# Kernel tuning notes

Hardware: AMD Instinct MI355X
Metric: run time of the kernel (lower is better)

## Reference

```python
import jax, jax.numpy as jnp
import numpy as np

HEADS = 8
DIM_HEAD = 64
DIM_INNER = HEADS * DIM_HEAD  # 512
SCALE = DIM_HEAD ** -0.5
B, N, D = 8, 512, 512
NEG = -1e9


def setup_inputs() -> dict:
    key = jax.random.key(0)
    ks = jax.random.split(key, 12)
    inp = {}
    for i in range(3):
        inp[f"x{i}"] = jax.random.normal(ks[i], (B, N, D), dtype=jnp.float32)
        inp[f"m{i}"] = jax.random.randint(ks[3 + i], (B, N), 0, 2).astype(bool)
        inp[f"Wqkv{i}"] = jax.random.normal(ks[6 + i], (D, 3 * DIM_INNER), dtype=jnp.float32) * 0.02
        inp[f"Wout{i}"] = jax.random.normal(ks[9 + i], (DIM_INNER, D), dtype=jnp.float32) * 0.02
    return inp


def _split_heads(t):
    # [b, n, h*d] -> [b, h, n, d]
    b, n, _ = t.shape
    return t.reshape(b, n, HEADS, DIM_HEAD).transpose(0, 2, 1, 3)


def _forward(xs, masks, Wqkvs, Wouts):
    qs, ks, vs = [], [], []
    for x, W in zip(xs, Wqkvs):
        q, k, v = jnp.split(x @ W, 3, axis=-1)
        qs.append(_split_heads(q))
        ks.append(_split_heads(k))
        vs.append(_split_heads(v))
    K = jnp.concatenate(ks, axis=2)  # [b, h, 3n, d]
    V = jnp.concatenate(vs, axis=2)
    outs = []
    for q, m, Wo in zip(qs, masks, Wouts):
        dots = jnp.einsum('bhnd,bhmd->bhnm', q, K) * SCALE
        # original masks whole query rows: masked_fill(~mask[:, None, :, None], -1e9)
        dots = jnp.where(m[:, None, :, None], dots, NEG)
        attn = jax.nn.softmax(dots, axis=-1)  # dropout is identity at eval
        o = jnp.einsum('bhnm,bhmd->bhnd', attn, V)
        o = o.transpose(0, 2, 1, 3).reshape(q.shape[0], q.shape[2], DIM_INNER)
        outs.append(o @ Wo)
    return tuple(outs)


def reference(x0, x1, x2, m0, m1, m2, Wqkv0, Wqkv1, Wqkv2, Wout0, Wout1, Wout2):
    return _forward((x0, x1, x2), (m0, m1, m2), (Wqkv0, Wqkv1, Wqkv2), (Wout0, Wout1, Wout2))
```

## Files before the change

### kernel.cpp

```cpp
#include <hip/hip_runtime.h>
#include <cstdint>
#include <cstddef>

#define NEGV  -1.0e9f
#define QSCALE 0.18033688011112042f

typedef _Float16 h8 __attribute__((ext_vector_type(8)));
typedef _Float16 h4 __attribute__((ext_vector_type(4)));
typedef float    f4 __attribute__((ext_vector_type(4)));


static __device__ inline h8 cvt8(float4 a, float4 b) {
    h8 r = { (_Float16)a.x, (_Float16)a.y, (_Float16)a.z, (_Float16)a.w,
             (_Float16)b.x, (_Float16)b.y, (_Float16)b.z, (_Float16)b.w };
    return r;
}

__global__ __launch_bounds__(256) void tr_cvt(
    const float* __restrict__ s0, const float* __restrict__ s1, const float* __restrict__ s2,
    _Float16* __restrict__ dst, int R, int C)
{
    const int mod = blockIdx.z;
    const float* __restrict__ s = (mod == 0) ? s0 : ((mod == 1) ? s1 : s2);
    _Float16* __restrict__ d = dst + (size_t)mod * R * C;
    const int c0 = blockIdx.x * 32, r0 = blockIdx.y * 32;
    __shared__ float tile[32][33];
    const int tr = threadIdx.x >> 3;
    const int tc = (threadIdx.x & 7) * 4;
    float4 v = *reinterpret_cast<const float4*>(&s[(size_t)(r0 + tr) * C + c0 + tc]);
    tile[tr][tc + 0] = v.x; tile[tr][tc + 1] = v.y; tile[tr][tc + 2] = v.z; tile[tr][tc + 3] = v.w;
    __syncthreads();
    h4 o = { (_Float16)tile[tc + 0][tr], (_Float16)tile[tc + 1][tr],
             (_Float16)tile[tc + 2][tr], (_Float16)tile[tc + 3][tr] };
    *reinterpret_cast<h4*>(&d[(size_t)(c0 + tr) * R + r0 + tc]) = o;
}

__global__ __launch_bounds__(256) void qkv_gemm_f16(
    const float* __restrict__ x0, const float* __restrict__ x1, const float* __restrict__ x2,
    const _Float16* __restrict__ Wqt,
    _Float16* __restrict__ Qh, _Float16* __restrict__ Kh, _Float16* __restrict__ Vt)
{
    const int mod = blockIdx.z;
    const float* __restrict__ A = (mod == 0) ? x0 : ((mod == 1) ? x1 : x2);
    const _Float16* __restrict__ Bw = Wqt + (size_t)mod * 1536 * 512;

    __shared__ _Float16 smem[2 * 128 * 40];
    _Float16* As = smem;
    _Float16* Bs = smem + 128 * 40;

    const int t = threadIdx.x;
    const int brow = blockIdx.x * 128, bcol = blockIdx.y * 128;
    const int w = t >> 6, l = t & 63;
    const int wr = (w >> 1) * 64, wc = (w & 1) * 64;
    const int lr = l & 15, lk = (l >> 4) * 8, lg = l >> 4;

    const int sm0 = t >> 2, skk = (t & 3) * 8, sm1 = sm0 + 64;

    f4 acc[4][4] = {};
    float4 axr[2][2];
    h8 brg[2];

    axr[0][0] = *reinterpret_cast<const float4*>(&A[(size_t)(brow + sm0) * 512 + skk]);
    axr[0][1] = *reinterpret_cast<const float4*>(&A[(size_t)(brow + sm0) * 512 + skk + 4]);
    axr[1][0] = *reinterpret_cast<const float4*>(&A[(size_t)(brow + sm1) * 512 + skk]);
    axr[1][1] = *reinterpret_cast<const float4*>(&A[(size_t)(brow + sm1) * 512 + skk + 4]);
    brg[0] = *reinterpret_cast<const h8*>(&Bw[(size_t)(bcol + sm0) * 512 + skk]);
    brg[1] = *reinterpret_cast<const h8*>(&Bw[(size_t)(bcol + sm1) * 512 + skk]);
    *reinterpret_cast<h8*>(&As[sm0 * 40 + skk]) = cvt8(axr[0][0], axr[0][1]);
    *reinterpret_cast<h8*>(&As[sm1 * 40 + skk]) = cvt8(axr[1][0], axr[1][1]);
    *reinterpret_cast<h8*>(&Bs[sm0 * 40 + skk]) = brg[0];
    *reinterpret_cast<h8*>(&Bs[sm1 * 40 + skk]) = brg[1];

    for (int k0 = 0; k0 < 512; k0 += 32) {
        __syncthreads();
        const bool more = (k0 + 32) < 512;
        if (more) {
            const int kn = k0 + 32 + skk;
            axr[0][0] = *reinterpret_cast<const float4*>(&A[(size_t)(brow + sm0) * 512 + kn]);
            axr[0][1] = *reinterpret_cast<const float4*>(&A[(size_t)(brow + sm0) * 512 + kn + 4]);
            axr[1][0] = *reinterpret_cast<const float4*>(&A[(size_t)(brow + sm1) * 512 + kn]);
            axr[1][1] = *reinterpret_cast<const float4*>(&A[(size_t)(brow + sm1) * 512 + kn + 4]);
            brg[0] = *reinterpret_cast<const h8*>(&Bw[(size_t)(bcol + sm0) * 512 + k0 + 32 + skk]);
            brg[1] = *reinterpret_cast<const h8*>(&Bw[(size_t)(bcol + sm1) * 512 + k0 + 32 + skk]);
        }
        h8 af[4], bf[4];
#pragma unroll
        for (int m = 0; m < 4; m++)
            af[m] = *reinterpret_cast<h8*>(&As[(wr + m * 16 + lr) * 40 + lk]);
#pragma unroll
        for (int n = 0; n < 4; n++)
            bf[n] = *reinterpret_cast<h8*>(&Bs[(wc + n * 16 + lr) * 40 + lk]);
        __builtin_amdgcn_s_setprio(1);
#pragma unroll
        for (int m = 0; m < 4; m++)
#pragma unroll
            for (int n = 0; n < 4; n++)
                acc[m][n] = __builtin_amdgcn_mfma_f32_16x16x32_f16(af[m], bf[n], acc[m][n], 0, 0, 0);
        __builtin_amdgcn_s_setprio(0);
        __syncthreads();
        if (more) {
            *reinterpret_cast<h8*>(&As[sm0 * 40 + skk]) = cvt8(axr[0][0], axr[0][1]);
            *reinterpret_cast<h8*>(&As[sm1 * 40 + skk]) = cvt8(axr[1][0], axr[1][1]);
            *reinterpret_cast<h8*>(&Bs[sm0 * 40 + skk]) = brg[0];
            *reinterpret_cast<h8*>(&Bs[sm1 * 40 + skk]) = brg[1];
        }
    }

    const int sec = bcol >> 9;
    const int b = brow >> 9;
    const int nbase = brow & 511;
    const int cbase = bcol - (sec << 9);

    if (sec == 2) {
#pragma unroll
        for (int m = 0; m < 4; m++) {
            const int n = nbase + wr + m * 16 + lg * 4;
#pragma unroll
            for (int nn = 0; nn < 4; nn++) {
                const int cis = cbase + wc + nn * 16 + lr;
                const int hh = cis >> 6, d = cis & 63;
                h4 pv = { (_Float16)acc[m][nn][0], (_Float16)acc[m][nn][1],
                          (_Float16)acc[m][nn][2], (_Float16)acc[m][nn][3] };
                *reinterpret_cast<h4*>(&Vt[(((size_t)b * 8 + hh) * 64 + d) * 1536 + mod * 512 + n]) = pv;
            }
        }
    } else {
        const float scl = (sec == 0) ? QSCALE : 1.0f;
        _Float16 (*Ts)[136] = reinterpret_cast<_Float16(*)[136]>(smem);
#pragma unroll
        for (int pass = 0; pass < 2; pass++) {
            __syncthreads();
            if ((w >> 1) == pass) {
#pragma unroll
                for (int m = 0; m < 4; m++)
#pragma unroll
                    for (int nn = 0; nn < 4; nn++)
#pragma unroll
                        for (int reg = 0; reg < 4; reg++)
                            Ts[m * 16 + lg * 4 + reg][wc + nn * 16 + lr] =
                                (_Float16)(acc[m][nn][reg] * scl);
            }
            __syncthreads();
#pragma unroll
            for (int it = 0; it < 4; it++) {
                const int idx = t + it * 256;
                const int r = idx >> 4, c = (idx & 15) * 8;
                h8 v = *reinterpret_cast<h8*>(&Ts[r][c]);
                const int n = nbase + pass * 64 + r;
                const int cis = cbase + c;
                const int hh = cis >> 6, d = cis & 63;
                if (sec == 0)
                    *reinterpret_cast<h8*>(&Qh[((((size_t)mod * 8 + b) * 8 + hh) * 512 + n) * 64 + d]) = v;
                else
                    *reinterpret_cast<h8*>(&Kh[(((size_t)b * 8 + hh) * 1536 + mod * 512 + n) * 64 + d]) = v;
            }
        }
    }
}

__global__ __launch_bounds__(512) void attn_f16(
    const _Float16* __restrict__ Qh, const _Float16* __restrict__ Kh, const _Float16* __restrict__ Vt,
    const int* __restrict__ m0, const int* __restrict__ m1, const int* __restrict__ m2,
    _Float16* __restrict__ Oh)
{
    const int mod = blockIdx.z;
    const int bh = blockIdx.x, b = bh >> 3, h = bh & 7;
    const int q0 = blockIdx.y * 128;

    __shared__ _Float16 Ks[64 * 72];
    __shared__ _Float16 Vs[64 * 72];
    __shared__ _Float16 Ps[128 * 72];

    const int t = threadIdx.x, w = t >> 6, l = t & 63;
    const int lr = l & 15, lg = l >> 4, lk = lg * 8;

    const _Float16* __restrict__ Qp = Qh + ((((size_t)mod * 8 + b) * 8 + h) * 512 + q0 + w * 16) * 64;
    h8 qf0 = *reinterpret_cast<const h8*>(&Qp[(size_t)lr * 64 + lk]);
    h8 qf1 = *reinterpret_cast<const h8*>(&Qp[(size_t)lr * 64 + 32 + lk]);

    const int* __restrict__ mk = (mod == 0) ? m0 : ((mod == 1) ? m1 : m2);
    const bool msk = mk[b * 512 + q0 + w * 16 + lr] != 0;

    float mrow = -3.0e38f, lsum = 0.f;
    f4 o[4] = {};

    const int sr = t >> 3, skk = (t & 7) * 8;
    const _Float16* __restrict__ kSrc = Kh + (size_t)bh * 1536 * 64 + (size_t)sr * 64 + skk;
    const _Float16* __restrict__ vSrc = Vt + (size_t)bh * 64 * 1536 + (size_t)sr * 1536 + skk;
    _Float16* kDst = &Ks[sr * 72 + skk];
    _Float16* vDst = &Vs[sr * 72 + skk];

    h8 krg = *reinterpret_cast<const h8*>(kSrc);
    h8 vrg = *reinterpret_cast<const h8*>(vSrc);
    *reinterpret_cast<h8*>(kDst) = krg;
    *reinterpret_cast<h8*>(vDst) = vrg;

    for (int c0 = 0; c0 < 1536; c0 += 64) {
        __syncthreads();
        const bool more = (c0 + 64) < 1536;
        if (more) {
            krg = *reinterpret_cast<const h8*>(kSrc + (size_t)(c0 + 64) * 64);
            vrg = *reinterpret_cast<const h8*>(vSrc + (c0 + 64));
        }

        f4 st[4] = {};
        __builtin_amdgcn_s_setprio(1);
#pragma unroll
        for (int kb = 0; kb < 4; kb++) {
            h8 ka0 = *reinterpret_cast<h8*>(&Ks[(kb * 16 + lr) * 72 + lk]);
            h8 ka1 = *reinterpret_cast<h8*>(&Ks[(kb * 16 + lr) * 72 + 32 + lk]);
            st[kb] = __builtin_amdgcn_mfma_f32_16x16x32_f16(ka0, qf0, st[kb], 0, 0, 0);
            st[kb] = __builtin_amdgcn_mfma_f32_16x16x32_f16(ka1, qf1, st[kb], 0, 0, 0);
        }
        __builtin_amdgcn_s_setprio(0);

        if (!msk) {
#pragma unroll
            for (int kb = 0; kb < 4; kb++) { st[kb][0] = NEGV; st[kb][1] = NEGV; st[kb][2] = NEGV; st[kb][3] = NEGV; }
        }
        float cm = fmaxf(fmaxf(fmaxf(st[0][0], st[0][1]), fmaxf(st[0][2], st[0][3])),
                         fmaxf(fmaxf(st[1][0], st[1][1]), fmaxf(st[1][2], st[1][3])));
        cm = fmaxf(cm, fmaxf(fmaxf(fmaxf(st[2][0], st[2][1]), fmaxf(st[2][2], st[2][3])),
                             fmaxf(fmaxf(st[3][0], st[3][1]), fmaxf(st[3][2], st[3][3]))));
        cm = fmaxf(cm, __shfl_xor(cm, 16));
        cm = fmaxf(cm, __shfl_xor(cm, 32));

        if (!__all(cm <= mrow + 8.0f)) {
            const float mn = fmaxf(mrow, cm);
            const float sc = __builtin_amdgcn_exp2f(mrow - mn);
            mrow = mn;
            lsum *= sc;
#pragma unroll
            for (int dg = 0; dg < 4; dg++) o[dg] *= sc;
        }

        float rs = 0.f;
#pragma unroll
        for (int kb = 0; kb < 4; kb++) {
            const float p0 = __builtin_amdgcn_exp2f(st[kb][0] - mrow);
            const float p1 = __builtin_amdgcn_exp2f(st[kb][1] - mrow);
            const float p2 = __builtin_amdgcn_exp2f(st[kb][2] - mrow);
            const float p3 = __builtin_amdgcn_exp2f(st[kb][3] - mrow);
            rs += (p0 + p1) + (p2 + p3);
            h4 ph = { (_Float16)p0, (_Float16)p1, (_Float16)p2, (_Float16)p3 };
            *reinterpret_cast<h4*>(&Ps[(w * 16 + lr) * 72 + kb * 16 + lg * 4]) = ph;
        }
        rs += __shfl_xor(rs, 16);
        rs += __shfl_xor(rs, 32);
        lsum += rs;

        __builtin_amdgcn_s_setprio(1);
#pragma unroll
        for (int kb2 = 0; kb2 < 2; kb2++) {
            h8 pa = *reinterpret_cast<h8*>(&Ps[(w * 16 + lr) * 72 + kb2 * 32 + lk]);
#pragma unroll
            for (int dg = 0; dg < 4; dg++) {
                h8 va = *reinterpret_cast<h8*>(&Vs[(dg * 16 + lr) * 72 + kb2 * 32 + lk]);
                o[dg] = __builtin_amdgcn_mfma_f32_16x16x32_f16(va, pa, o[dg], 0, 0, 0);
            }
        }
        __builtin_amdgcn_s_setprio(0);

        __syncthreads();
        if (more) {
            *reinterpret_cast<h8*>(kDst) = krg;
            *reinterpret_cast<h8*>(vDst) = vrg;
        }
    }

    const float inv = 1.f / lsum;
    const size_t row = (size_t)mod * 4096 + b * 512 + q0 + w * 16 + lr;
#pragma unroll
    for (int dg = 0; dg < 4; dg++) {
        h4 ov = { (_Float16)(o[dg][0] * inv), (_Float16)(o[dg][1] * inv),
                  (_Float16)(o[dg][2] * inv), (_Float16)(o[dg][3] * inv) };
        *reinterpret_cast<h4*>(&Oh[row * 512 + h * 64 + dg * 16 + lg * 4]) = ov;
    }
}

__global__ __launch_bounds__(256) void out_gemm_f16(
    const _Float16* __restrict__ Oh, const _Float16* __restrict__ Wot,
    float* __restrict__ out)
{
    const int mod = blockIdx.z;
    const _Float16* __restrict__ A  = Oh  + (size_t)mod * 4096 * 512;
    const _Float16* __restrict__ Bw = Wot + (size_t)mod * 512 * 512;
    float* __restrict__ C = out + (size_t)mod * 4096 * 512;

    __shared__ _Float16 As[128 * 40];
    __shared__ _Float16 Bs[128 * 40];

    const int t = threadIdx.x;
    const int brow = blockIdx.x * 128, bcol = blockIdx.y * 128;
    const int w = t >> 6, l = t & 63;
    const int wr = (w >> 1) * 64, wc = (w & 1) * 64;
    const int lr = l & 15, lk = (l >> 4) * 8, lg = l >> 4;

    const int sm0 = t >> 2, skk = (t & 3) * 8, sm1 = sm0 + 64;

    f4 acc[4][4] = {};
    h8 arg[2], brg[2];

    arg[0] = *reinterpret_cast<const h8*>(&A [(size_t)(brow + sm0) * 512 + skk]);
    arg[1] = *reinterpret_cast<const h8*>(&A [(size_t)(brow + sm1) * 512 + skk]);
    brg[0] = *reinterpret_cast<const h8*>(&Bw[(size_t)(bcol + sm0) * 512 + skk]);
    brg[1] = *reinterpret_cast<const h8*>(&Bw[(size_t)(bcol + sm1) * 512 + skk]);
    *reinterpret_cast<h8*>(&As[sm0 * 40 + skk]) = arg[0];
    *reinterpret_cast<h8*>(&As[sm1 * 40 + skk]) = arg[1];
    *reinterpret_cast<h8*>(&Bs[sm0 * 40 + skk]) = brg[0];
    *reinterpret_cast<h8*>(&Bs[sm1 * 40 + skk]) = brg[1];

    for (int k0 = 0; k0 < 512; k0 += 32) {
        __syncthreads();
        const bool more = (k0 + 32) < 512;
        if (more) {
            const int kn = k0 + 32 + skk;
            arg[0] = *reinterpret_cast<const h8*>(&A [(size_t)(brow + sm0) * 512 + kn]);
            arg[1] = *reinterpret_cast<const h8*>(&A [(size_t)(brow + sm1) * 512 + kn]);
            brg[0] = *reinterpret_cast<const h8*>(&Bw[(size_t)(bcol + sm0) * 512 + kn]);
            brg[1] = *reinterpret_cast<const h8*>(&Bw[(size_t)(bcol + sm1) * 512 + kn]);
        }
        h8 af[4], bf[4];
#pragma unroll
        for (int m = 0; m < 4; m++)
            af[m] = *reinterpret_cast<h8*>(&As[(wr + m * 16 + lr) * 40 + lk]);
#pragma unroll
        for (int n = 0; n < 4; n++)
            bf[n] = *reinterpret_cast<h8*>(&Bs[(wc + n * 16 + lr) * 40 + lk]);
        __builtin_amdgcn_s_setprio(1);
#pragma unroll
        for (int m = 0; m < 4; m++)
#pragma unroll
            for (int n = 0; n < 4; n++)
                acc[m][n] = __builtin_amdgcn_mfma_f32_16x16x32_f16(af[m], bf[n], acc[m][n], 0, 0, 0);
        __builtin_amdgcn_s_setprio(0);
        __syncthreads();
        if (more) {
            *reinterpret_cast<h8*>(&As[sm0 * 40 + skk]) = arg[0];
            *reinterpret_cast<h8*>(&As[sm1 * 40 + skk]) = arg[1];
            *reinterpret_cast<h8*>(&Bs[sm0 * 40 + skk]) = brg[0];
            *reinterpret_cast<h8*>(&Bs[sm1 * 40 + skk]) = brg[1];
        }
    }

#pragma unroll
    for (int m = 0; m < 4; m++) {
        const int rloc = wr + m * 16 + lg * 4;
#pragma unroll
        for (int reg = 0; reg < 4; reg++) {
            const size_t base = (size_t)(brow + rloc + reg) * 512 + bcol;
#pragma unroll
            for (int nn = 0; nn < 4; nn++)
                C[base + wc + nn * 16 + lr] = acc[m][nn][reg];
        }
    }
}

extern "C" void kernel_launch(void* const* d_in, const int* in_sizes, int n_in,
                              void* d_out, int out_size, void* d_ws, size_t ws_size,
                              hipStream_t stream)
{
    const float* x0  = (const float*)d_in[0];
    const int*   m0  = (const int*)  d_in[1];
    const float* Wq0 = (const float*)d_in[2];
    const float* Wo0 = (const float*)d_in[3];
    const float* x1  = (const float*)d_in[4];
    const int*   m1  = (const int*)  d_in[5];
    const float* Wq1 = (const float*)d_in[6];
    const float* Wo1 = (const float*)d_in[7];
    const float* x2  = (const float*)d_in[8];
    const int*   m2  = (const int*)  d_in[9];
    const float* Wq2 = (const float*)d_in[10];
    const float* Wo2 = (const float*)d_in[11];

    _Float16* Wqt = (_Float16*)d_ws;
    _Float16* Wot = Wqt + 2359296;
    _Float16* Qh  = Wot + 786432;
    _Float16* Kh  = Qh  + 6291456;
    _Float16* Vt  = Kh  + 6291456;
    _Float16* Oh  = Vt  + 6291456;

    tr_cvt<<<dim3(48, 16, 3), 256, 0, stream>>>(Wq0, Wq1, Wq2, Wqt, 512, 1536);
    tr_cvt<<<dim3(16, 16, 3), 256, 0, stream>>>(Wo0, Wo1, Wo2, Wot, 512, 512);

    qkv_gemm_f16<<<dim3(32, 12, 3), 256, 0, stream>>>(x0, x1, x2, Wqt, Qh, Kh, Vt);
    attn_f16    <<<dim3(64, 4, 3), 512, 0, stream>>>(Qh, Kh, Vt, m0, m1, m2, Oh);
    out_gemm_f16<<<dim3(32, 4, 3), 256, 0, stream>>>(Oh, Wot, (float*)d_out);
}
```

Measured before the change: 230.7 us.

## Coalesce V and output stores via LDS, merge weight converts, shrink attention blocks

```diff
diff --git a/kernel.cpp b/kernel.cpp
--- a/kernel.cpp
+++ b/kernel.cpp
@@ -16,14 +16,26 @@
     return r;
 }
 
-__global__ __launch_bounds__(256) void tr_cvt(
-    const float* __restrict__ s0, const float* __restrict__ s1, const float* __restrict__ s2,
-    _Float16* __restrict__ dst, int R, int C)
+__global__ __launch_bounds__(256) void wt_cvt(
+    const float* __restrict__ q0, const float* __restrict__ q1, const float* __restrict__ q2,
+    const float* __restrict__ o0, const float* __restrict__ o1, const float* __restrict__ o2,
+    _Float16* __restrict__ Wqt, _Float16* __restrict__ Wot)
 {
     const int mod = blockIdx.z;
-    const float* __restrict__ s = (mod == 0) ? s0 : ((mod == 1) ? s1 : s2);
-    _Float16* __restrict__ d = dst + (size_t)mod * R * C;
-    const int c0 = blockIdx.x * 32, r0 = blockIdx.y * 32;
+    const int flat = blockIdx.x;
+    const float* s;
+    _Float16* d;
+    int C, bx, by;
+    if (flat < 768) {
+        C = 1536; bx = flat % 48; by = flat / 48;
+        s = (mod == 0) ? q0 : ((mod == 1) ? q1 : q2);
+        d = Wqt + (size_t)mod * 1536 * 512;
+    } else {
+        C = 512; bx = (flat - 768) % 16; by = (flat - 768) / 16;
+        s = (mod == 0) ? o0 : ((mod == 1) ? o1 : o2);
+        d = Wot + (size_t)mod * 512 * 512;
+    }
+    const int c0 = bx * 32, r0 = by * 32;
     __shared__ float tile[32][33];
     const int tr = threadIdx.x >> 3;
     const int tc = (threadIdx.x & 7) * 4;
@@ -32,7 +44,7 @@
     __syncthreads();
     h4 o = { (_Float16)tile[tc + 0][tr], (_Float16)tile[tc + 1][tr],
              (_Float16)tile[tc + 2][tr], (_Float16)tile[tc + 3][tr] };
-    *reinterpret_cast<h4*>(&d[(size_t)(c0 + tr) * R + r0 + tc]) = o;
+    *reinterpret_cast<h4*>(&d[(size_t)(c0 + tr) * 512 + r0 + tc]) = o;
 }
 
 __global__ __launch_bounds__(256) void qkv_gemm_f16(
@@ -112,17 +124,29 @@
     const int cbase = bcol - (sec << 9);
 
     if (sec == 2) {
-#pragma unroll
-        for (int m = 0; m < 4; m++) {
-            const int n = nbase + wr + m * 16 + lg * 4;
-#pragma unroll
-            for (int nn = 0; nn < 4; nn++) {
-                const int cis = cbase + wc + nn * 16 + lr;
-                const int hh = cis >> 6, d = cis & 63;
-                h4 pv = { (_Float16)acc[m][nn][0], (_Float16)acc[m][nn][1],
-                          (_Float16)acc[m][nn][2], (_Float16)acc[m][nn][3] };
-                *reinterpret_cast<h4*>(&Vt[(((size_t)b * 8 + hh) * 64 + d) * 1536 + mod * 512 + n]) = pv;
+        _Float16 (*Tv)[136] = reinterpret_cast<_Float16(*)[136]>(smem);
+#pragma unroll
+        for (int pass = 0; pass < 2; pass++) {
+            __syncthreads();
+            if ((w & 1) == pass) {
+#pragma unroll
+                for (int m = 0; m < 4; m++)
+#pragma unroll
+                    for (int nn = 0; nn < 4; nn++)
+#pragma unroll
+                        for (int reg = 0; reg < 4; reg++)
+                            Tv[nn * 16 + lr][wr + m * 16 + lg * 4 + reg] =
+                                (_Float16)acc[m][nn][reg];
             }
+            __syncthreads();
+            const int c  = t >> 2;
+            const int kb = (t & 3) * 32;
+            const int cis = cbase + pass * 64 + c;
+            const int hh = cis >> 6, d = cis & 63;
+            _Float16* dst = &Vt[(((size_t)b * 8 + hh) * 64 + d) * 1536 + mod * 512 + nbase + kb];
+#pragma unroll
+            for (int u = 0; u < 4; u++)
+                *reinterpret_cast<h8*>(&dst[u * 8]) = *reinterpret_cast<h8*>(&Tv[c][kb + u * 8]);
         }
     } else {
         const float scl = (sec == 0) ? QSCALE : 1.0f;
@@ -158,18 +182,18 @@
     }
 }
 
-__global__ __launch_bounds__(512) void attn_f16(
+__global__ __launch_bounds__(256) void attn_f16(
     const _Float16* __restrict__ Qh, const _Float16* __restrict__ Kh, const _Float16* __restrict__ Vt,
     const int* __restrict__ m0, const int* __restrict__ m1, const int* __restrict__ m2,
     _Float16* __restrict__ Oh)
 {
     const int mod = blockIdx.z;
     const int bh = blockIdx.x, b = bh >> 3, h = bh & 7;
-    const int q0 = blockIdx.y * 128;
+    const int q0 = blockIdx.y * 64;
 
     __shared__ _Float16 Ks[64 * 72];
     __shared__ _Float16 Vs[64 * 72];
-    __shared__ _Float16 Ps[128 * 72];
+    __shared__ _Float16 Ps[64 * 72];
 
     const int t = threadIdx.x, w = t >> 6, l = t & 63;
     const int lr = l & 15, lg = l >> 4, lk = lg * 8;
@@ -184,23 +208,29 @@
     float mrow = -3.0e38f, lsum = 0.f;
     f4 o[4] = {};
 
-    const int sr = t >> 3, skk = (t & 7) * 8;
-    const _Float16* __restrict__ kSrc = Kh + (size_t)bh * 1536 * 64 + (size_t)sr * 64 + skk;
-    const _Float16* __restrict__ vSrc = Vt + (size_t)bh * 64 * 1536 + (size_t)sr * 1536 + skk;
-    _Float16* kDst = &Ks[sr * 72 + skk];
-    _Float16* vDst = &Vs[sr * 72 + skk];
-
-    h8 krg = *reinterpret_cast<const h8*>(kSrc);
-    h8 vrg = *reinterpret_cast<const h8*>(vSrc);
-    *reinterpret_cast<h8*>(kDst) = krg;
-    *reinterpret_cast<h8*>(vDst) = vrg;
+    const int sr0 = t >> 3, skk = (t & 7) * 8, sr1 = sr0 + 32;
+    const _Float16* __restrict__ kSrc = Kh + (size_t)bh * 1536 * 64 + skk;
+    const _Float16* __restrict__ vSrc = Vt + (size_t)bh * 64 * 1536 + skk;
+
+    h8 krg[2], vrg[2];
+    krg[0] = *reinterpret_cast<const h8*>(kSrc + (size_t)sr0 * 64);
+    krg[1] = *reinterpret_cast<const h8*>(kSrc + (size_t)sr1 * 64);
+    vrg[0] = *reinterpret_cast<const h8*>(vSrc + (size_t)sr0 * 1536);
+    vrg[1] = *reinterpret_cast<const h8*>(vSrc + (size_t)sr1 * 1536);
+    *reinterpret_cast<h8*>(&Ks[sr0 * 72 + skk]) = krg[0];
+    *reinterpret_cast<h8*>(&Ks[sr1 * 72 + skk]) = krg[1];
+    *reinterpret_cast<h8*>(&Vs[sr0 * 72 + skk]) = vrg[0];
+    *reinterpret_cast<h8*>(&Vs[sr1 * 72 + skk]) = vrg[1];
 
     for (int c0 = 0; c0 < 1536; c0 += 64) {
         __syncthreads();
         const bool more = (c0 + 64) < 1536;
         if (more) {
-            krg = *reinterpret_cast<const h8*>(kSrc + (size_t)(c0 + 64) * 64);
-            vrg = *reinterpret_cast<const h8*>(vSrc + (c0 + 64));
+            const int cn = c0 + 64;
+            krg[0] = *reinterpret_cast<const h8*>(kSrc + (size_t)(cn + sr0) * 64);
+            krg[1] = *reinterpret_cast<const h8*>(kSrc + (size_t)(cn + sr1) * 64);
+            vrg[0] = *reinterpret_cast<const h8*>(vSrc + (size_t)sr0 * 1536 + cn);
+            vrg[1] = *reinterpret_cast<const h8*>(vSrc + (size_t)sr1 * 1536 + cn);
         }
 
         f4 st[4] = {};
@@ -263,8 +293,10 @@
 
         __syncthreads();
         if (more) {
-            *reinterpret_cast<h8*>(kDst) = krg;
-            *reinterpret_cast<h8*>(vDst) = vrg;
+            *reinterpret_cast<h8*>(&Ks[sr0 * 72 + skk]) = krg[0];
+            *reinterpret_cast<h8*>(&Ks[sr1 * 72 + skk]) = krg[1];
+            *reinterpret_cast<h8*>(&Vs[sr0 * 72 + skk]) = vrg[0];
+            *reinterpret_cast<h8*>(&Vs[sr1 * 72 + skk]) = vrg[1];
         }
     }
 
@@ -287,8 +319,9 @@
     const _Float16* __restrict__ Bw = Wot + (size_t)mod * 512 * 512;
     float* __restrict__ C = out + (size_t)mod * 4096 * 512;
 
-    __shared__ _Float16 As[128 * 40];
-    __shared__ _Float16 Bs[128 * 40];
+    __shared__ _Float16 smem[2 * 128 * 40];
+    _Float16* As = smem;
+    _Float16* Bs = smem + 128 * 40;
 
     const int t = threadIdx.x;
     const int brow = blockIdx.x * 128, bcol = blockIdx.y * 128;
@@ -343,16 +376,27 @@
         }
     }
 
-#pragma unroll
-    for (int m = 0; m < 4; m++) {
-        const int rloc = wr + m * 16 + lg * 4;
-#pragma unroll
-        for (int reg = 0; reg < 4; reg++) {
-            const size_t base = (size_t)(brow + rloc + reg) * 512 + bcol;
-#pragma unroll
-            for (int nn = 0; nn < 4; nn++)
-                C[base + wc + nn * 16 + lr] = acc[m][nn][reg];
-        }
+    float (*Tf)[132] = reinterpret_cast<float(*)[132]>(smem);
+#pragma unroll
+    for (int pass = 0; pass < 4; pass++) {
+        __syncthreads();
+        if ((w >> 1) == (pass >> 1)) {
+#pragma unroll
+            for (int mm = 0; mm < 2; mm++) {
+                const int m = (pass & 1) * 2 + mm;
+#pragma unroll
+                for (int nn = 0; nn < 4; nn++)
+#pragma unroll
+                    for (int reg = 0; reg < 4; reg++)
+                        Tf[mm * 16 + lg * 4 + reg][wc + nn * 16 + lr] = acc[m][nn][reg];
+            }
+        }
+        __syncthreads();
+        const int r = t >> 3, cb = (t & 7) * 16;
+        float* dst = &C[(size_t)(brow + pass * 32 + r) * 512 + bcol + cb];
+#pragma unroll
+        for (int u = 0; u < 4; u++)
+            *reinterpret_cast<float4*>(&dst[u * 4]) = *reinterpret_cast<float4*>(&Tf[r][cb + u * 4]);
     }
 }
 
@@ -380,10 +424,8 @@
     _Float16* Vt  = Kh  + 6291456;
     _Float16* Oh  = Vt  + 6291456;
 
-    tr_cvt<<<dim3(48, 16, 3), 256, 0, stream>>>(Wq0, Wq1, Wq2, Wqt, 512, 1536);
-    tr_cvt<<<dim3(16, 16, 3), 256, 0, stream>>>(Wo0, Wo1, Wo2, Wot, 512, 512);
-
+    wt_cvt<<<dim3(1024, 1, 3), 256, 0, stream>>>(Wq0, Wq1, Wq2, Wo0, Wo1, Wo2, Wqt, Wot);
     qkv_gemm_f16<<<dim3(32, 12, 3), 256, 0, stream>>>(x0, x1, x2, Wqt, Qh, Kh, Vt);
-    attn_f16    <<<dim3(64, 4, 3), 512, 0, stream>>>(Qh, Kh, Vt, m0, m1, m2, Oh);
+    attn_f16    <<<dim3(64, 8, 3), 256, 0, stream>>>(Qh, Kh, Vt, m0, m1, m2, Oh);
     out_gemm_f16<<<dim3(32, 4, 3), 256, 0, stream>>>(Oh, Wot, (float*)d_out);
 }
```

Measured after the change: 254.4 us. +10.3%, slower.
